# Kernel optimization log

Measured on AMD Instinct MI355X. Metric: run time of the kernel, lower is better.

## Reference

```python
import jax, jax.numpy as jnp
import numpy as np

# Module hyper-parameters (from init_kwargs)
NDIM = 2
KSIZE = [3, 3]            # must be odd per ConvSP checks
DILATION = [0.05, 0.05]
RADIUS = 0.1
C_IN, C_OUT = 64, 64
B, N = 2, 2048


def _offsets():
    # Kernel-cell center offsets relative to the particle, row-major over dims
    # (matches the cartesian ordering of the original C extension).
    axes = [(np.arange(k) - (k - 1) / 2.0) * d for k, d in zip(KSIZE, DILATION)]
    grids = np.meshgrid(*axes, indexing='ij')
    return np.stack([g.reshape(-1) for g in grids], axis=-1).astype(np.float32)  # [ncells, D]


def setup_inputs() -> dict:
    key = jax.random.key(0)
    k1, k2, k3, k4, k5, k6 = jax.random.split(key, 6)
    pos = jax.random.uniform(k1, (B, N, NDIM), dtype=jnp.float32)          # coords in [0,1]^D
    invmass = jax.random.uniform(k2, (B, N), dtype=jnp.float32) * 0.9 + 0.1  # avoid 1/0
    locs = jnp.concatenate([pos, invmass[..., None]], axis=-1)             # [B,N,D+1]
    data = jax.random.normal(k3, (B, C_IN, N), dtype=jnp.float32)
    density = jax.random.uniform(k4, (B, N), dtype=jnp.float32) + 0.5      # strictly positive
    ncells = int(np.prod(KSIZE))
    weight = jax.random.normal(k5, (C_OUT, C_IN, ncells), dtype=jnp.float32) * 0.05
    bias = jax.random.normal(k6, (C_OUT,), dtype=jnp.float32) * 0.05
    return {"locs": locs, "data": data, "density": density, "weight": weight, "bias": bias}


def _convsp(locs, data, density, weight, bias):
    # SPH interpolation at each kernel-cell query point r_{i,k} = x_i + off_k:
    #   field[b,c,i,k] = sum_j (m_j / rho_j) * data[b,c,j] * W(|x_j - r_{i,k}|, RADIUS)
    # with m_j = 1/invmass_j, then a 1x1-style contraction with weight over (c,k).
    pos = locs[..., :NDIM]                               # [B,N,D]
    invmass = locs[..., NDIM]                            # [B,N]
    coef = 1.0 / (invmass * density)                     # m_j / rho_j, [B,N]
    dcoef = data * coef[:, None, :]                      # [B,C,N]
    diff = pos[:, :, None, :] - pos[:, None, :, :]       # x_i - x_j, [B,N,N,D]
    r2 = RADIUS * RADIUS
    knorm = 315.0 / (64.0 * np.pi * RADIUS ** 9)         # poly6 smoothing kernel norm
    offs = _offsets()                                    # [ncells, D]
    bsz, n = pos.shape[0], pos.shape[1]
    out = jnp.broadcast_to(bias[None, :, None], (bsz, weight.shape[0], n))
    for k in range(offs.shape[0]):                       # fixed small ncells=9 loop
        # |x_j - x_i - off| == |(x_i - x_j) + off|
        d2 = jnp.sum((diff + offs[k]) ** 2, axis=-1)     # [B,N,N] (i = query, j = neighbor)
        w = jnp.where(d2 < r2, (r2 - d2) ** 3, 0.0) * knorm
        field = jnp.einsum('bcj,bij->bci', dcoef, w)     # gather-weighted average
        out = out + jnp.einsum('oc,bci->boi', weight[:, :, k], field)
    return out


def reference(locs, data, density, weight, bias):
    return _convsp(locs, data, density, weight, bias)
```

## Files before the change

### kernel.cpp

```cpp
#include <hip/hip_runtime.h>
#include <hip/hip_bf16.h>
#include <stdint.h>

#define BATCH 2
#define NPTS  2048
#define CIN   64
#define COUT  64
#define NCELL 9

#define KNORM 1.5666851e9f
#define R2 0.01f

typedef __attribute__((ext_vector_type(8))) __bf16 bf16x8;
typedef __attribute__((ext_vector_type(4))) float  f32x4;

union B8 { uint4 u; bf16x8 v; };

typedef __attribute__((address_space(3))) uint8_t        lds_t;
typedef const __attribute__((address_space(1))) uint8_t  glb_t;

static __device__ __forceinline__ unsigned pk2(float a, float b) {
    union { __hip_bfloat162 h; unsigned u; } cv;
    cv.h = __float22bfloat162_rn(make_float2(a, b));
    return cv.u;
}


__global__ __launch_bounds__(256) void prep_kernel(
    const float* __restrict__ locs, const float* __restrict__ data,
    const float* __restrict__ density, const float* __restrict__ weight,
    const float* __restrict__ bias,
    float2* __restrict__ posT, uint16_t* __restrict__ dC,
    uint16_t* __restrict__ WB, float* __restrict__ out)
{
    const int tid = threadIdx.x;
    const int g = blockIdx.x;
    if (g < 256) {
        int e = g * 256 + tid;
        int j4 = e & 511, bc = e >> 9;
        int b = bc >> 6;
        float4 dv = *(const float4*)(data + bc * 2048 + j4 * 4);
        float4 de = *(const float4*)(density + b * 2048 + j4 * 4);
        int jb = (b * 2048 + j4 * 4) * 3 + 2;
        float m0 = locs[jb], m1 = locs[jb + 3], m2 = locs[jb + 6], m3 = locs[jb + 9];
        float v0 = dv.x / (m0 * de.x) * KNORM;
        float v1 = dv.y / (m1 * de.y) * KNORM;
        float v2 = dv.z / (m2 * de.z) * KNORM;
        float v3 = dv.w / (m3 * de.w) * KNORM;
        *(uint2*)(dC + bc * 2048 + j4 * 4) = make_uint2(pk2(v0, v1), pk2(v2, v3));
    } else if (g < 272) {
        int jj = (g - 256) * 256 + tid;
        posT[jj] = make_float2(locs[jj * 3], locs[jj * 3 + 1]);
    } else if (g < 272 + NCELL) {
        int cell = g - 272;
        for (int it = 0; it < 16; it++) {
            int e = it * 256 + tid;
            int ks = e >> 11, ob = (e >> 9) & 3, lane = (e >> 3) & 63, jj = e & 7;
            int o = ob * 16 + (lane & 15);
            int c = ks * 32 + ((lane >> 4) & 3) * 8 + jj;
            union { __hip_bfloat16 h; uint16_t u; } cv;
            cv.h = __float2bfloat16(weight[(o * 64 + c) * 9 + cell]);
            WB[cell * 4096 + e] = cv.u;
        }
    } else {
        const int gb = g - (272 + NCELL);
#pragma unroll
        for (int r = 0; r < 2; r++) {
            int e4 = (gb * 512 + r * 256 + tid) * 4;
            float bv = bias[(e4 >> 11) & 63];
            *(float4*)(out + e4) = make_float4(bv, bv, bv, bv);
        }
    }
}

__global__ __launch_bounds__(256, 4) void conv_kernel(
    const float2* __restrict__ posT, const uint16_t* __restrict__ dC,
    const uint16_t* __restrict__ WB, float* __restrict__ out)
{
    __shared__ uint16_t db[2][2048];
    __shared__ float    sft[4 * 16 * 68];

    const int tid  = threadIdx.x;
    const int lane = tid & 63;
    const int wid  = tid >> 6;
    const int cl   = lane & 15;
    const int quad = lane >> 4;
    const int bx   = blockIdx.x;
    const int b    = bx >> 9;
    const int i0   = ((bx >> 2) & 127) * 16;
    const int jh   = bx & 3;
    const int jb0  = jh * 512;

    const int hw = ((bx >> 8) + bx) & 3;
    const int r  = (wid - hw) & 3;
    const int c0 = (r == 0) ? 0 : (1 + r * 2);
    const int nc = (r == 0) ? 3 : 2;

    float cxr[3], cyr[3], ccr[3];
#pragma unroll
    for (int ci = 0; ci < 3; ci++) {
        int k = c0 + (ci < nc ? ci : 0);
        float ox = (float)(k / 3 - 1) * 0.05f;
        float oy = (float)(k % 3 - 1) * 0.05f;
        cxr[ci] = -2.0f * ox;
        cyr[ci] = -2.0f * oy;
        ccr[ci] = -(ox * ox + oy * oy);
    }

    const float2 pI = posT[b * 2048 + i0 + cl];

    f32x4 acc[3][4];
#pragma unroll
    for (int ci = 0; ci < 3; ci++)
#pragma unroll
        for (int nb = 0; nb < 4; nb++) acc[ci][nb] = (f32x4){0.f, 0.f, 0.f, 0.f};

    const uint16_t* srcbase =
        dC + (b * 64 + wid * 16 + (lane >> 2)) * 2048 + jb0 + (lane & 3) * 8;

#define STAGE(n, buf)                                                         \
    __builtin_amdgcn_global_load_lds((glb_t*)(srcbase + (n) * 32),            \
                                     (lds_t*)(&db[buf][wid * 512]), 16, 0, 0)

    STAGE(0, 0);

    for (int n = 0; n < 16; n++) {
        __syncthreads();
        if (n < 15) STAGE(n + 1, (n + 1) & 1);
        const int buf = n & 1;

        B8 bf[4];
#pragma unroll
        for (int nb = 0; nb < 4; nb++)
            bf[nb].u = *(const uint4*)&db[buf][(nb * 16 + cl) * 32 + quad * 8];

        const float4* pp = (const float4*)(posT + b * 2048 + jb0 + n * 32 + quad * 8);
        float4 q0 = pp[0], q1 = pp[1], q2 = pp[2], q3 = pp[3];
        float dxv[8], dyv[8], sv[8];
        dxv[0] = pI.x - q0.x; dyv[0] = pI.y - q0.y;
        dxv[1] = pI.x - q0.z; dyv[1] = pI.y - q0.w;
        dxv[2] = pI.x - q1.x; dyv[2] = pI.y - q1.y;
        dxv[3] = pI.x - q1.z; dyv[3] = pI.y - q1.w;
        dxv[4] = pI.x - q2.x; dyv[4] = pI.y - q2.y;
        dxv[5] = pI.x - q2.z; dyv[5] = pI.y - q2.w;
        dxv[6] = pI.x - q3.x; dyv[6] = pI.y - q3.y;
        dxv[7] = pI.x - q3.z; dyv[7] = pI.y - q3.w;
#pragma unroll
        for (int p = 0; p < 8; p++)
            sv[p] = fmaf(-dyv[p], dyv[p], fmaf(-dxv[p], dxv[p], R2));

#pragma unroll
        for (int ci = 0; ci < 3; ci++) {
            if (ci < nc) {
                const float cx = cxr[ci], cy = cyr[ci], cc = ccr[ci];
                float w[8];
#pragma unroll
                for (int p = 0; p < 8; p++) {
                    float t  = fmaf(cx, dxv[p], fmaf(cy, dyv[p], sv[p] + cc));
                    float mt = fmaxf(t, 0.0f);
                    w[p] = (mt * mt) * mt;
                }
                B8 af;
                af.u = make_uint4(pk2(w[0], w[1]), pk2(w[2], w[3]),
                                  pk2(w[4], w[5]), pk2(w[6], w[7]));
#pragma unroll
                for (int nb = 0; nb < 4; nb++)
                    acc[ci][nb] = __builtin_amdgcn_mfma_f32_16x16x32_bf16(
                        af.v, bf[nb].v, acc[ci][nb], 0, 0, 0);
            }
        }
    }

    float* scr = &sft[wid * (16 * 68)];
    f32x4 acc2[4];
#pragma unroll
    for (int ob = 0; ob < 4; ob++) acc2[ob] = (f32x4){0.f, 0.f, 0.f, 0.f};

#pragma unroll
    for (int ci = 0; ci < 3; ci++) {
        if (ci < nc) {
#pragma unroll
            for (int nb = 0; nb < 4; nb++)
#pragma unroll
                for (int rr = 0; rr < 4; rr++)
                    scr[(quad * 4 + rr) * 68 + nb * 16 + cl] = acc[ci][nb][rr];
            int k = c0 + ci;
#pragma unroll
            for (int ks = 0; ks < 2; ks++) {
                const float* fp = &scr[cl * 68 + ks * 32 + quad * 8];
                float4 lo = *(const float4*)fp;
                float4 hi = *(const float4*)(fp + 4);
                B8 af;
                af.u = make_uint4(pk2(lo.x, lo.y), pk2(lo.z, lo.w),
                                  pk2(hi.x, hi.y), pk2(hi.z, hi.w));
#pragma unroll
                for (int ob = 0; ob < 4; ob++) {
                    B8 wf;
                    wf.u = *(const uint4*)(WB + k * 4096 + (ks * 4 + ob) * 512 + lane * 8);
                    acc2[ob] = __builtin_amdgcn_mfma_f32_16x16x32_bf16(
                        af.v, wf.v, acc2[ob], 0, 0, 0);
                }
            }
        }
    }

    __syncthreads();
#pragma unroll
    for (int ob = 0; ob < 4; ob++)
#pragma unroll
        for (int rr = 0; rr < 4; rr++)
            scr[(quad * 4 + rr) * 68 + ob * 16 + cl] = acc2[ob][rr];
    __syncthreads();

    {
        const int i  = tid & 15;
        const int og = tid >> 4;
        float4 s0 = *(const float4*)&sft[0 * 1088 + i * 68 + og * 4];
        float4 s1 = *(const float4*)&sft[1 * 1088 + i * 68 + og * 4];
        float4 s2 = *(const float4*)&sft[2 * 1088 + i * 68 + og * 4];
        float4 s3 = *(const float4*)&sft[3 * 1088 + i * 68 + og * 4];
        float v0 = s0.x + s1.x + s2.x + s3.x;
        float v1 = s0.y + s1.y + s2.y + s3.y;
        float v2 = s0.z + s1.z + s2.z + s3.z;
        float v3 = s0.w + s1.w + s2.w + s3.w;
        float* ob_ = out + (b * 64 + og * 4) * 2048 + i0 + i;
        unsafeAtomicAdd(ob_ + 0 * 2048, v0);
        unsafeAtomicAdd(ob_ + 1 * 2048, v1);
        unsafeAtomicAdd(ob_ + 2 * 2048, v2);
        unsafeAtomicAdd(ob_ + 3 * 2048, v3);
    }
#undef STAGE
}

extern "C" void kernel_launch(void* const* d_in, const int* in_sizes, int n_in,
                              void* d_out, int out_size, void* d_ws, size_t ws_size,
                              hipStream_t stream)
{
    const float* locs    = (const float*)d_in[0];
    const float* data    = (const float*)d_in[1];
    const float* density = (const float*)d_in[2];
    const float* weight  = (const float*)d_in[3];
    const float* bias    = (const float*)d_in[4];
    float* out = (float*)d_out;

    float2*   posT = (float2*)d_ws;
    uint16_t* dC   = (uint16_t*)((char*)d_ws + 32768);
    uint16_t* WB   = (uint16_t*)((char*)d_ws + 32768 + 524288);

    prep_kernel<<<272 + NCELL + 128, 256, 0, stream>>>(
        locs, data, density, weight, bias, posT, dC, WB, out);
    conv_kernel<<<BATCH * 128 * 4, 256, 0, stream>>>(posT, dC, WB, out);
}
```

Baseline: 90.91 us.

## Specialize per-wave cell constants and double the staged chunk per barrier

Each wave's kernel-cell offsets become compile-time constants through per-role branches, so FMAs with zero offset terms are skipped. Cells are regrouped so the three-cell wave handles the centre and two axis cells, which need the fewest FMAs. The LDS staging buffer now holds two 32-column chunks per stage, halving the number of barriers and loop iterations. The cost is more code, since every role branch is unrolled, and doubled LDS use for the data buffer, which may affect occupancy.

Measured after the change: 102.0 us. 1.12x slower.

```diff
diff --git a/kernel.cpp b/kernel.cpp
--- a/kernel.cpp
+++ b/kernel.cpp
@@ -77,7 +77,7 @@
     const float2* __restrict__ posT, const uint16_t* __restrict__ dC,
     const uint16_t* __restrict__ WB, float* __restrict__ out)
 {
-    __shared__ uint16_t db[2][2048];
+    __shared__ uint16_t db[2][2][2048];
     __shared__ float    sft[4 * 16 * 68];
 
     const int tid  = threadIdx.x;
@@ -93,21 +93,9 @@
 
     const int hw = ((bx >> 8) + bx) & 3;
     const int r  = (wid - hw) & 3;
-    const int c0 = (r == 0) ? 0 : (1 + r * 2);
-    const int nc = (r == 0) ? 3 : 2;
-
-    float cxr[3], cyr[3], ccr[3];
-#pragma unroll
-    for (int ci = 0; ci < 3; ci++) {
-        int k = c0 + (ci < nc ? ci : 0);
-        float ox = (float)(k / 3 - 1) * 0.05f;
-        float oy = (float)(k % 3 - 1) * 0.05f;
-        cxr[ci] = -2.0f * ox;
-        cyr[ci] = -2.0f * oy;
-        ccr[ci] = -(ox * ox + oy * oy);
-    }
 
     const float2 pI = posT[b * 2048 + i0 + cl];
+    const float2* pbase = posT + b * 2048 + jb0;
 
     f32x4 acc[3][4];
 #pragma unroll
@@ -118,58 +106,86 @@
     const uint16_t* srcbase =
         dC + (b * 64 + wid * 16 + (lane >> 2)) * 2048 + jb0 + (lane & 3) * 8;
 
-#define STAGE(n, buf)                                                         \
+#define STAGE(n, buf, half)                                                   \
     __builtin_amdgcn_global_load_lds((glb_t*)(srcbase + (n) * 32),            \
-                                     (lds_t*)(&db[buf][wid * 512]), 16, 0, 0)
-
-    STAGE(0, 0);
-
-    for (int n = 0; n < 16; n++) {
+                                     (lds_t*)(&db[buf][half][wid * 512]), 16, 0, 0)
+
+#define CELL(CI, CX, CY, CC, HASX, HASY)                                      \
+    {                                                                         \
+        float w_[8];                                                          \
+        _Pragma("unroll")                                                     \
+        for (int p = 0; p < 8; p++) {                                         \
+            float t = sv[p];                                                  \
+            if (HASY) t = fmaf((CY), dyv[p], t);                              \
+            if (HASX) t = fmaf((CX), dxv[p], t);                              \
+            if ((HASX) || (HASY)) t += (CC);                                  \
+            float mt = fmaxf(t, 0.0f);                                        \
+            w_[p] = (mt * mt) * mt;                                           \
+        }                                                                     \
+        B8 af;                                                                \
+        af.u = make_uint4(pk2(w_[0], w_[1]), pk2(w_[2], w_[3]),               \
+                          pk2(w_[4], w_[5]), pk2(w_[6], w_[7]));              \
+        _Pragma("unroll")                                                     \
+        for (int nb = 0; nb < 4; nb++)                                        \
+            acc[CI][nb] = __builtin_amdgcn_mfma_f32_16x16x32_bf16(            \
+                af.v, bf[nb].v, acc[CI][nb], 0, 0, 0);                        \
+    }
+
+    STAGE(0, 0, 0);
+    STAGE(1, 0, 1);
+
+    for (int it = 0; it < 8; it++) {
         __syncthreads();
-        if (n < 15) STAGE(n + 1, (n + 1) & 1);
-        const int buf = n & 1;
-
-        B8 bf[4];
-#pragma unroll
-        for (int nb = 0; nb < 4; nb++)
-            bf[nb].u = *(const uint4*)&db[buf][(nb * 16 + cl) * 32 + quad * 8];
-
-        const float4* pp = (const float4*)(posT + b * 2048 + jb0 + n * 32 + quad * 8);
-        float4 q0 = pp[0], q1 = pp[1], q2 = pp[2], q3 = pp[3];
-        float dxv[8], dyv[8], sv[8];
-        dxv[0] = pI.x - q0.x; dyv[0] = pI.y - q0.y;
-        dxv[1] = pI.x - q0.z; dyv[1] = pI.y - q0.w;
-        dxv[2] = pI.x - q1.x; dyv[2] = pI.y - q1.y;
-        dxv[3] = pI.x - q1.z; dyv[3] = pI.y - q1.w;
-        dxv[4] = pI.x - q2.x; dyv[4] = pI.y - q2.y;
-        dxv[5] = pI.x - q2.z; dyv[5] = pI.y - q2.w;
-        dxv[6] = pI.x - q3.x; dyv[6] = pI.y - q3.y;
-        dxv[7] = pI.x - q3.z; dyv[7] = pI.y - q3.w;
-#pragma unroll
-        for (int p = 0; p < 8; p++)
-            sv[p] = fmaf(-dyv[p], dyv[p], fmaf(-dxv[p], dxv[p], R2));
-
-#pragma unroll
-        for (int ci = 0; ci < 3; ci++) {
-            if (ci < nc) {
-                const float cx = cxr[ci], cy = cyr[ci], cc = ccr[ci];
-                float w[8];
-#pragma unroll
-                for (int p = 0; p < 8; p++) {
-                    float t  = fmaf(cx, dxv[p], fmaf(cy, dyv[p], sv[p] + cc));
-                    float mt = fmaxf(t, 0.0f);
-                    w[p] = (mt * mt) * mt;
-                }
-                B8 af;
-                af.u = make_uint4(pk2(w[0], w[1]), pk2(w[2], w[3]),
-                                  pk2(w[4], w[5]), pk2(w[6], w[7]));
-#pragma unroll
-                for (int nb = 0; nb < 4; nb++)
-                    acc[ci][nb] = __builtin_amdgcn_mfma_f32_16x16x32_bf16(
-                        af.v, bf[nb].v, acc[ci][nb], 0, 0, 0);
+        const int buf = it & 1;
+        if (it < 7) { STAGE(2 * it + 2, buf ^ 1, 0); STAGE(2 * it + 3, buf ^ 1, 1); }
+
+#pragma unroll
+        for (int half = 0; half < 2; half++) {
+            const int n = 2 * it + half;
+
+            B8 bf[4];
+#pragma unroll
+            for (int nb = 0; nb < 4; nb++)
+                bf[nb].u = *(const uint4*)&db[buf][half][(nb * 16 + cl) * 32 + quad * 8];
+
+            const float4* pp = (const float4*)(pbase + n * 32 + quad * 8);
+            float4 q0 = pp[0], q1 = pp[1], q2 = pp[2], q3 = pp[3];
+            float dxv[8], dyv[8], sv[8];
+            dxv[0] = pI.x - q0.x; dyv[0] = pI.y - q0.y;
+            dxv[1] = pI.x - q0.z; dyv[1] = pI.y - q0.w;
+            dxv[2] = pI.x - q1.x; dyv[2] = pI.y - q1.y;
+            dxv[3] = pI.x - q1.z; dyv[3] = pI.y - q1.w;
+            dxv[4] = pI.x - q2.x; dyv[4] = pI.y - q2.y;
+            dxv[5] = pI.x - q2.z; dyv[5] = pI.y - q2.w;
+            dxv[6] = pI.x - q3.x; dyv[6] = pI.y - q3.y;
+            dxv[7] = pI.x - q3.z; dyv[7] = pI.y - q3.w;
+#pragma unroll
+            for (int p = 0; p < 8; p++)
+                sv[p] = fmaf(-dyv[p], dyv[p], fmaf(-dxv[p], dxv[p], R2));
+
+            if (r == 0) {
+                CELL(0,  0.1f,  0.1f, -0.005f,  1, 1);
+                CELL(1,  0.1f, -0.1f, -0.005f,  1, 1);
+            } else if (r == 1) {
+                CELL(0, -0.1f,  0.1f, -0.005f,  1, 1);
+                CELL(1, -0.1f, -0.1f, -0.005f,  1, 1);
+            } else if (r == 2) {
+                CELL(0,  0.1f,  0.0f, -0.0025f, 1, 0);
+                CELL(1,  0.0f,  0.1f, -0.0025f, 0, 1);
+                CELL(2,  0.0f,  0.0f,  0.0f,    0, 0);
+            } else {
+                CELL(0,  0.0f, -0.1f, -0.0025f, 0, 1);
+                CELL(1, -0.1f,  0.0f, -0.0025f, 1, 0);
             }
         }
     }
+
+    const int nc = (r == 2) ? 3 : 2;
+    int kcs[3];
+    if (r == 0)      { kcs[0] = 0; kcs[1] = 2; kcs[2] = 0; }
+    else if (r == 1) { kcs[0] = 6; kcs[1] = 8; kcs[2] = 0; }
+    else if (r == 2) { kcs[0] = 1; kcs[1] = 3; kcs[2] = 4; }
+    else             { kcs[0] = 5; kcs[1] = 7; kcs[2] = 0; }
 
     float* scr = &sft[wid * (16 * 68)];
     f32x4 acc2[4];
@@ -184,7 +200,7 @@
 #pragma unroll
                 for (int rr = 0; rr < 4; rr++)
                     scr[(quad * 4 + rr) * 68 + nb * 16 + cl] = acc[ci][nb][rr];
-            int k = c0 + ci;
+            int k = kcs[ci];
 #pragma unroll
             for (int ks = 0; ks < 2; ks++) {
                 const float* fp = &scr[cl * 68 + ks * 32 + quad * 8];
@@ -230,6 +246,7 @@
         unsafeAtomicAdd(ob_ + 3 * 2048, v3);
     }
 #undef STAGE
+#undef CELL
 }
 
 extern "C" void kernel_launch(void* const* d_in, const int* in_sizes, int n_in,
```
